# Performance work log

Measured on AMD Instinct MI355X. Metric: run time of the kernel, lower is better.

Reference implementation:

```python
import jax, jax.numpy as jnp
import numpy as np

N_LEVELS = 16
N_FEATS = 2
MIN_RES = 16
MAX_RES = 2048
LOG2_T = 19
T = 1 << LOG2_T  # 524288 hash-table entries per level
B = np.exp((np.log(MAX_RES) - np.log(MIN_RES)) / (N_LEVELS - 1))  # per-level scale ~1.3819
PRIME_Y = np.uint32(2654435761)  # tcnn 2D spatial-hash prime (x prime is 1)
MASK = jnp.uint32(T - 1)


def hash_encode(uv, table):
    """Multiresolution hash-grid encoding (tcnn HashGrid, 2D, bilinear).
    uv: [N,2] in [0,1); table: [L,T,F]. Returns [N, L*F]."""
    outs = []
    for l in range(N_LEVELS):
        scale = MIN_RES * (B ** l) - 1.0          # tcnn grid_scale
        res = int(np.ceil(scale)) + 1             # tcnn grid_resolution
        dense = (res * res) <= T                  # small levels are dense grids
        pos = uv * jnp.float32(scale) + jnp.float32(0.5)
        pg_f = jnp.floor(pos)
        frac = pos - pg_f                          # [N,2] bilinear weights
        pg = pg_f.astype(jnp.uint32)

        def corner_idx(ox, oy):
            x = pg[:, 0] + jnp.uint32(ox)
            y = pg[:, 1] + jnp.uint32(oy)
            if dense:
                return (x + y * jnp.uint32(res)) & MASK
            return (x ^ (y * PRIME_Y)) & MASK

        fx = frac[:, 0:1]
        fy = frac[:, 1:2]
        tl = table[l]
        feat = ((1.0 - fx) * (1.0 - fy) * tl[corner_idx(0, 0)]
                + fx * (1.0 - fy) * tl[corner_idx(1, 0)]
                + (1.0 - fx) * fy * tl[corner_idx(0, 1)]
                + fx * fy * tl[corner_idx(1, 1)])
        outs.append(feat)
    return jnp.concatenate(outs, axis=-1)  # [N, 32]


def mlp(x, w0, w1, w2):
    # FullyFusedMLP: no biases, ReLU hidden, Sigmoid output
    h = jax.nn.relu(x @ w0)
    h = jax.nn.relu(h @ w1)
    return jax.nn.sigmoid(h @ w2)  # [N, 3]


def setup_inputs() -> dict:
    key = jax.random.key(0)
    ks = jax.random.split(key, 5)
    N = 2_097_152
    uv = jax.random.uniform(ks[0], (N, 2), jnp.float32)
    # tcnn HashGrid init: uniform in [-1e-4, 1e-4]
    table = jax.random.uniform(ks[1], (N_LEVELS, T, N_FEATS), jnp.float32, -1e-4, 1e-4)
    w0 = jax.random.normal(ks[2], (32, 64), jnp.float32) * jnp.float32(1.0 / np.sqrt(32))
    w1 = jax.random.normal(ks[3], (64, 64), jnp.float32) * jnp.float32(1.0 / np.sqrt(64))
    w2 = jax.random.normal(ks[4], (64, 3), jnp.float32) * jnp.float32(1.0 / np.sqrt(64))
    return {"uv": uv, "table": table, "w0": w0, "w1": w1, "w2": w2}


def reference(uv, table, w0, w1, w2):
    return mlp(hash_encode(uv, table), w0, w1, w2)
```

## Files before the change

kernel.cpp:

```cpp
#include <hip/hip_runtime.h>
#include <math.h>
#include <stdint.h>

#define NLV 16
#define LOG2T 19
#define TSZ (1u << LOG2T)
#define TMASK (TSZ - 1u)
#define PRIME_Y 2654435761u

#define NFRAG 14
#define WPF_USHORTS (NFRAG * 64 * 8)

#define NCOARSE 512
#define P1_PTS 8192
#define P2_CAP 5120

struct NGPParams {
    float scale[NLV];
    unsigned res[NLV];
    unsigned hashed_mask;
};

struct __align__(8) pairld { float x, y, z, w; };

typedef __attribute__((ext_vector_type(8))) short bf16x8;
typedef __attribute__((ext_vector_type(4))) float f32x4;

__device__ inline ushort bf16_rn(float f) {
    uint32_t u = __float_as_uint(f);
    return (ushort)((u + 0x7FFFu + ((u >> 16) & 1u)) >> 16);
}
__device__ inline uint32_t pack_bf16(float a, float b) {
    uint32_t ua = __float_as_uint(a);
    uint32_t ub = __float_as_uint(b);
    uint32_t lo = (ua + 0x7FFFu + ((ua >> 16) & 1u)) >> 16;
    uint32_t hi = (ub + 0x7FFFu + ((ub >> 16) & 1u)) & 0xFFFF0000u;
    return lo | hi;
}
__device__ inline uint32_t pack_trunc(float a, float b) {
    return __builtin_amdgcn_perm(__float_as_uint(a), __float_as_uint(b), 0x07060302u);
}
__device__ inline unsigned coarse_of(float2 v) {
    unsigned b = (unsigned)(v.y * 512.f); return b > 511u ? 511u : b;
}
__device__ inline unsigned fine_of(float2 v) {
    unsigned b = (unsigned)(v.x * 256.f); return b > 255u ? 255u : b;
}
__device__ inline int xcd_swz(int orig, int nwg) {
    const int q = nwg >> 3, r = nwg & 7;
    const int xcd = orig & 7, k = orig >> 3;
    return (xcd < r ? xcd * (q + 1) : r * (q + 1) + (xcd - r) * q) + k;
}

__global__ __launch_bounds__(256) void ngp_prep_wfrag(
    const float* __restrict__ w0, const float* __restrict__ w1,
    const float* __restrict__ w2, ushort* __restrict__ wpf)
{
    const int t = threadIdx.x;
    for (int i = 0; i < 4; ++i) {
        const int e = t + 256 * i;
        if (e >= NFRAG * 64) continue;
        const int f = e >> 6, lane = e & 63;
        const int g4 = lane >> 4, r16 = lane & 15;
        ushort v[8];
        if (f < 4) {
            const int n = f * 16 + r16, k0 = 8 * g4;
            #pragma unroll
            for (int j = 0; j < 8; ++j) v[j] = bf16_rn(w0[(k0 + j) * 64 + n]);
        } else if (f < 12) {
            const int q = f - 4;
            const int n = (q >> 1) * 16 + r16, k0 = (q & 1) * 32 + 8 * g4;
            #pragma unroll
            for (int j = 0; j < 8; ++j) v[j] = bf16_rn(w1[(k0 + j) * 64 + n]);
        } else {
            const int n = r16, k0 = (f - 12) * 32 + 8 * g4;
            #pragma unroll
            for (int j = 0; j < 8; ++j)
                v[j] = (n < 3) ? bf16_rn(w2[(k0 + j) * 3 + n]) : (ushort)0;
        }
        #pragma unroll
        for (int j = 0; j < 8; ++j) wpf[e * 8 + j] = v[j];
    }
}

__global__ __launch_bounds__(1024) void ngp_hist512(
    const float2* __restrict__ uv, uint32_t* __restrict__ hist, int n)
{
    __shared__ unsigned int h[NCOARSE];
    const int t = threadIdx.x;
    if (t < NCOARSE) h[t] = 0;
    __syncthreads();
    const int b0 = blockIdx.x * P1_PTS;
    #pragma unroll
    for (int k = 0; k < 8; ++k) {
        const int i = b0 + t + k * 1024;
        if (i < n) atomicAdd(&h[coarse_of(uv[i])], 1u);
    }
    __syncthreads();
    if (t < NCOARSE && h[t]) atomicAdd(&hist[t], h[t]);
}

__global__ __launch_bounds__(512) void ngp_scan512(
    const uint32_t* __restrict__ hist, uint32_t* __restrict__ base,
    uint32_t* __restrict__ cursor)
{
    __shared__ unsigned int s[NCOARSE];
    const int t = threadIdx.x;
    const uint32_t mine = hist[t];
    s[t] = mine;
    __syncthreads();
    for (int off = 1; off < NCOARSE; off <<= 1) {
        uint32_t v = (t >= off) ? s[t - off] : 0u;
        __syncthreads();
        s[t] += v;
        __syncthreads();
    }
    const uint32_t excl = s[t] - mine;
    base[t] = excl;
    cursor[t] = excl;
}

__global__ __launch_bounds__(1024) void ngp_pass1(
    const float2* __restrict__ uv, uint32_t* __restrict__ cursor,
    float2* __restrict__ suv, uint32_t* __restrict__ perm, int n)
{
    __shared__ float2       spt[P1_PTS];
    __shared__ unsigned int sid[P1_PTS];
    __shared__ unsigned int hist[NCOARSE], lbase[NCOARSE], lcur[NCOARSE], gbase[NCOARSE];
    __shared__ unsigned int stot;

    const int t = threadIdx.x;
    const int b0 = blockIdx.x * P1_PTS;
    if (t < NCOARSE) hist[t] = 0;
    __syncthreads();

    float2 p[8]; unsigned pc[8];
    #pragma unroll
    for (int k = 0; k < 8; ++k) {
        const int i = b0 + t + k * 1024;
        if (i < n) {
            p[k] = uv[i];
            pc[k] = coarse_of(p[k]);
            atomicAdd(&hist[pc[k]], 1u);
        } else pc[k] = 0xFFFFFFFFu;
    }
    __syncthreads();
    if (t < NCOARSE) lbase[t] = hist[t];
    __syncthreads();
    for (int off = 1; off < NCOARSE; off <<= 1) {
        uint32_t v = 0;
        if (t < NCOARSE && t >= off) v = lbase[t - off];
        __syncthreads();
        if (t < NCOARSE) lbase[t] += v;
        __syncthreads();
    }
    if (t < NCOARSE) {
        const uint32_t excl = lbase[t] - hist[t];
        lcur[t] = excl;
        gbase[t] = atomicAdd(&cursor[t], hist[t]);
        lbase[t] = excl;
        if (t == NCOARSE - 1) stot = excl + hist[t];
    }
    __syncthreads();
    #pragma unroll
    for (int k = 0; k < 8; ++k) {
        if (pc[k] != 0xFFFFFFFFu) {
            const uint32_t r = atomicAdd(&lcur[pc[k]], 1u);
            spt[r] = p[k];
            sid[r] = (unsigned)(b0 + t + k * 1024);
        }
    }
    __syncthreads();
    const uint32_t tot = stot;
    for (uint32_t j = t; j < tot; j += 1024) {
        const float2 v = spt[j];
        const unsigned c = coarse_of(v);
        const uint32_t d = gbase[c] + (j - lbase[c]);
        suv[d] = v;
        perm[d] = sid[j];
    }
}

__global__ __launch_bounds__(1024) void ngp_pass2(
    const uint32_t* __restrict__ basev, const uint32_t* __restrict__ histv,
    float2* __restrict__ suv, uint32_t* __restrict__ perm)
{
    __shared__ float2       spt[P2_CAP];
    __shared__ unsigned int sid[P2_CAP];
    __shared__ unsigned int hist[256], lbase[256], lcur[256];

    const int b = blockIdx.x;
    const uint32_t lo = basev[b];
    const uint32_t cnt = histv[b];
    if (cnt > P2_CAP) return;
    const int t = threadIdx.x;
    if (t < 256) hist[t] = 0;
    __syncthreads();
    for (uint32_t j = t; j < cnt; j += 1024) {
        const float2 v = suv[lo + j];
        spt[j] = v; sid[j] = perm[lo + j];
        atomicAdd(&hist[fine_of(v)], 1u);
    }
    __syncthreads();
    if (t < 256) lbase[t] = hist[t];
    __syncthreads();
    for (int off = 1; off < 256; off <<= 1) {
        uint32_t v = 0;
        if (t < 256 && t >= off) v = lbase[t - off];
        __syncthreads();
        if (t < 256) lbase[t] += v;
        __syncthreads();
    }
    if (t < 256) lcur[t] = lbase[t] - hist[t];
    __syncthreads();
    for (uint32_t j = t; j < cnt; j += 1024) {
        const float2 v = spt[j];
        const uint32_t r = atomicAdd(&lcur[fine_of(v)], 1u);
        suv[lo + r] = v;
        perm[lo + r] = sid[j];
    }
}

__global__ __launch_bounds__(256) void ngp_encode2_kernel(
    const float2* __restrict__ pts,
    const float2* __restrict__ table,
    uint32_t* __restrict__ xt,
    NGPParams p, int n, int chunks2)
{
    const int bid = blockIdx.x;
    const int pass = bid / chunks2;
    const int chunk = xcd_swz(bid - pass * chunks2, chunks2);
    const int base = chunk * 512 + threadIdx.x;

    float2 xy[2];
    #pragma unroll
    for (int q = 0; q < 2; ++q) {
        int idx = base + q * 256;
        xy[q] = pts[idx < n ? idx : (n - 1)];
    }

    const int l0 = (pass == 0) ? 0 : (pass == 1 ? 10 : 10 + pass);
    const int l1 = (pass == 0) ? 9 : (pass == 1 ? 11 : 10 + pass);

    for (int l = l0; l <= l1; ++l) {
        const float s = p.scale[l];
        const unsigned res = p.res[l];
        const bool hashed = (p.hashed_mask >> l) & 1u;
        const float2* tl = table + ((size_t)l << LOG2T);

        #pragma unroll
        for (int q = 0; q < 2; ++q) {
            const float px = xy[q].x * s + 0.5f;
            const float py = xy[q].y * s + 0.5f;
            const float fpx = floorf(px), fpy = floorf(py);
            const float fx = px - fpx, fy = py - fpy;
            const unsigned x0 = (unsigned)fpx, y0 = (unsigned)fpy;

            float2 c00, c10, c01, c11;
            if (!hashed) {
                const unsigned b0 = x0 + y0 * res;
                const pairld q0 = *(const pairld*)(tl + b0);
                const pairld q1 = *(const pairld*)(tl + b0 + res);
                c00 = make_float2(q0.x, q0.y); c10 = make_float2(q0.z, q0.w);
                c01 = make_float2(q1.x, q1.y); c11 = make_float2(q1.z, q1.w);
            } else {
                const unsigned hy0 = y0 * PRIME_Y;
                const unsigned hy1 = (y0 + 1u) * PRIME_Y;
                if (!(x0 & 1u)) {
                    const unsigned i0 = (x0 ^ hy0) & TMASK;
                    const unsigned i2 = (x0 ^ hy1) & TMASK;
                    const pairld q0 = *(const pairld*)(tl + (i0 & ~1u));
                    const pairld q2 = *(const pairld*)(tl + (i2 & ~1u));
                    if (i0 & 1u) { c00 = make_float2(q0.z, q0.w); c10 = make_float2(q0.x, q0.y); }
                    else         { c00 = make_float2(q0.x, q0.y); c10 = make_float2(q0.z, q0.w); }
                    if (i2 & 1u) { c01 = make_float2(q2.z, q2.w); c11 = make_float2(q2.x, q2.y); }
                    else         { c01 = make_float2(q2.x, q2.y); c11 = make_float2(q2.z, q2.w); }
                } else {
                    c00 = tl[(x0 ^ hy0) & TMASK];
                    c10 = tl[((x0 + 1u) ^ hy0) & TMASK];
                    c01 = tl[(x0 ^ hy1) & TMASK];
                    c11 = tl[((x0 + 1u) ^ hy1) & TMASK];
                }
            }

            const float w00 = (1.f - fx) * (1.f - fy);
            const float w10 = fx * (1.f - fy);
            const float w01 = (1.f - fx) * fy;
            const float w11 = fx * fy;
            const float f0 = w00 * c00.x + w10 * c10.x + w01 * c01.x + w11 * c11.x;
            const float f1 = w00 * c00.y + w10 * c10.y + w01 * c01.y + w11 * c11.y;
            const int idx = base + q * 256;
            if (idx < n) xt[(size_t)l * n + idx] = pack_bf16(f0, f1);
        }
    }
}

__global__ __launch_bounds__(256, 4) void ngp_mlp_persist(
    const uint32_t* __restrict__ xt,
    const ushort* __restrict__ wpf,
    const uint32_t* __restrict__ perm,
    float* __restrict__ out, int n, int nchunks)
{
    __shared__ __align__(16) ushort H[256 * 72];

    const int t = threadIdx.x;
    const int lane = t & 63;
    const int w = t >> 6;
    const int g4 = lane >> 4;
    const int r16 = lane & 15;

    bf16x8 wf[NFRAG];
    #pragma unroll
    for (int f = 0; f < NFRAG; ++f)
        wf[f] = *(const bf16x8*)(wpf + (size_t)(f * 64 + lane) * 8);

    for (int c = blockIdx.x; c < nchunks; c += gridDim.x) {
        const int pbase = c << 8;
        #pragma unroll
        for (int mi = 0; mi < 4; ++mi) {
            const int plocal = (w * 4 + mi) * 16 + r16;
            int pg = pbase + plocal;
            pg = pg < n ? pg : n - 1;
            union { uint32_t u[4]; bf16x8 v; } cv;
            #pragma unroll
            for (int c4 = 0; c4 < 4; ++c4)
                cv.u[c4] = xt[(size_t)(4 * g4 + c4) * n + pg];
            f32x4 a[4];
            #pragma unroll
            for (int nt = 0; nt < 4; ++nt)
                a[nt] = __builtin_amdgcn_mfma_f32_16x16x32_bf16(
                    wf[nt], cv.v, (f32x4){0.f, 0.f, 0.f, 0.f}, 0, 0, 0);
            const int pl = plocal * 72;
            #pragma unroll
            for (int nt = 0; nt < 4; ++nt) {
                const uint32_t d0 = pack_trunc(fmaxf(a[nt][1], 0.f), fmaxf(a[nt][0], 0.f));
                const uint32_t d1 = pack_trunc(fmaxf(a[nt][3], 0.f), fmaxf(a[nt][2], 0.f));
                *(uint2*)&H[pl + nt * 16 + 4 * g4] = make_uint2(d0, d1);
            }
        }
        #pragma unroll
        for (int mi = 0; mi < 4; ++mi) {
            const int plocal = (w * 4 + mi) * 16 + r16;
            const int pl = plocal * 72;
            const bf16x8 bh0 = *(const bf16x8*)&H[pl + 8 * g4];
            const bf16x8 bh1 = *(const bf16x8*)&H[pl + 32 + 8 * g4];
            #pragma unroll
            for (int nt = 0; nt < 4; ++nt) {
                f32x4 acc = __builtin_amdgcn_mfma_f32_16x16x32_bf16(
                    wf[4 + nt * 2], bh0, (f32x4){0.f, 0.f, 0.f, 0.f}, 0, 0, 0);
                acc = __builtin_amdgcn_mfma_f32_16x16x32_bf16(
                    wf[4 + nt * 2 + 1], bh1, acc, 0, 0, 0);
                const uint32_t d0 = pack_trunc(fmaxf(acc[1], 0.f), fmaxf(acc[0], 0.f));
                const uint32_t d1 = pack_trunc(fmaxf(acc[3], 0.f), fmaxf(acc[2], 0.f));
                *(uint2*)&H[pl + nt * 16 + 4 * g4] = make_uint2(d0, d1);
            }
            const bf16x8 ch0 = *(const bf16x8*)&H[pl + 8 * g4];
            const bf16x8 ch1 = *(const bf16x8*)&H[pl + 32 + 8 * g4];
            f32x4 z = __builtin_amdgcn_mfma_f32_16x16x32_bf16(
                wf[12], ch0, (f32x4){0.f, 0.f, 0.f, 0.f}, 0, 0, 0);
            z = __builtin_amdgcn_mfma_f32_16x16x32_bf16(wf[13], ch1, z, 0, 0, 0);
            if (g4 == 0) {
                const int pgs = pbase + plocal;
                if (pgs < n) {
                    const int pg = perm ? (int)perm[pgs] : pgs;
                    #pragma unroll
                    for (int r = 0; r < 3; ++r)
                        out[(size_t)pg * 3 + r] = 1.f / (1.f + __expf(-z[r]));
                }
            }
        }
    }
}

__global__ __launch_bounds__(256) void ngp_fused_kernel(
    const float2* __restrict__ uv,
    const float2* __restrict__ table,
    const float4* __restrict__ w0,
    const float4* __restrict__ w1,
    const float*  __restrict__ w2,
    float* __restrict__ out,
    NGPParams p, int n)
{
    __shared__ float4 sw0[512];
    __shared__ float4 sw1[1024];
    __shared__ float  sw2[192];
    const int t = threadIdx.x;
    #pragma unroll
    for (int i = 0; i < 2; i++) sw0[t + 256 * i] = w0[t + 256 * i];
    #pragma unroll
    for (int i = 0; i < 4; i++) sw1[t + 256 * i] = w1[t + 256 * i];
    if (t < 192) sw2[t] = w2[t];
    __syncthreads();
    const int gi = blockIdx.x * 256 + t;
    if (gi >= n) return;
    const float2 xy = uv[gi];
    float feat[32];
    #pragma unroll
    for (int l = 0; l < NLV; l++) {
        const float s = p.scale[l];
        const unsigned res = p.res[l];
        const float px = xy.x * s + 0.5f;
        const float py = xy.y * s + 0.5f;
        const float fpx = floorf(px), fpy = floorf(py);
        const float fx = px - fpx, fy = py - fpy;
        const unsigned x0 = (unsigned)fpx, y0 = (unsigned)fpy;
        unsigned i00, i10, i01, i11;
        if (!((p.hashed_mask >> l) & 1u)) {
            const unsigned b = x0 + y0 * res;
            i00 = b & TMASK; i10 = (b + 1u) & TMASK;
            i01 = (b + res) & TMASK; i11 = (b + res + 1u) & TMASK;
        } else {
            const unsigned hy0 = y0 * PRIME_Y;
            const unsigned hy1 = (y0 + 1u) * PRIME_Y;
            i00 = (x0 ^ hy0) & TMASK; i10 = ((x0 + 1u) ^ hy0) & TMASK;
            i01 = (x0 ^ hy1) & TMASK; i11 = ((x0 + 1u) ^ hy1) & TMASK;
        }
        const float2* tl = table + ((size_t)l << LOG2T);
        const float2 c00 = tl[i00], c10 = tl[i10], c01 = tl[i01], c11 = tl[i11];
        const float w00 = (1.f - fx) * (1.f - fy);
        const float w10 = fx * (1.f - fy);
        const float w01 = (1.f - fx) * fy;
        const float w11 = fx * fy;
        feat[2 * l]     = w00 * c00.x + w10 * c10.x + w01 * c01.x + w11 * c11.x;
        feat[2 * l + 1] = w00 * c00.y + w10 * c10.y + w01 * c01.y + w11 * c11.y;
    }
    float2 h0[32];
    #pragma unroll
    for (int j = 0; j < 32; j++) h0[j] = make_float2(0.f, 0.f);
    #pragma unroll
    for (int k = 0; k < 32; k++) {
        const float f = feat[k];
        #pragma unroll
        for (int j = 0; j < 16; j++) {
            const float4 ww = sw0[k * 16 + j];
            h0[2 * j].x = fmaf(f, ww.x, h0[2 * j].x);
            h0[2 * j].y = fmaf(f, ww.y, h0[2 * j].y);
            h0[2 * j + 1].x = fmaf(f, ww.z, h0[2 * j + 1].x);
            h0[2 * j + 1].y = fmaf(f, ww.w, h0[2 * j + 1].y);
        }
    }
    #pragma unroll
    for (int j = 0; j < 32; j++) {
        h0[j].x = fmaxf(h0[j].x, 0.f);
        h0[j].y = fmaxf(h0[j].y, 0.f);
    }
    float2 h1[32];
    #pragma unroll
    for (int j = 0; j < 32; j++) h1[j] = make_float2(0.f, 0.f);
    #pragma unroll
    for (int k = 0; k < 64; k++) {
        const float f = (k & 1) ? h0[k >> 1].y : h0[k >> 1].x;
        #pragma unroll
        for (int j = 0; j < 16; j++) {
            const float4 ww = sw1[k * 16 + j];
            h1[2 * j].x = fmaf(f, ww.x, h1[2 * j].x);
            h1[2 * j].y = fmaf(f, ww.y, h1[2 * j].y);
            h1[2 * j + 1].x = fmaf(f, ww.z, h1[2 * j + 1].x);
            h1[2 * j + 1].y = fmaf(f, ww.w, h1[2 * j + 1].y);
        }
    }
    #pragma unroll
    for (int j = 0; j < 32; j++) {
        h1[j].x = fmaxf(h1[j].x, 0.f);
        h1[j].y = fmaxf(h1[j].y, 0.f);
    }
    float z0 = 0.f, z1 = 0.f, z2 = 0.f;
    #pragma unroll
    for (int k = 0; k < 64; k++) {
        const float f = (k & 1) ? h1[k >> 1].y : h1[k >> 1].x;
        z0 = fmaf(f, sw2[3 * k + 0], z0);
        z1 = fmaf(f, sw2[3 * k + 1], z1);
        z2 = fmaf(f, sw2[3 * k + 2], z2);
    }
    out[3 * gi + 0] = 1.f / (1.f + __expf(-z0));
    out[3 * gi + 1] = 1.f / (1.f + __expf(-z1));
    out[3 * gi + 2] = 1.f / (1.f + __expf(-z2));
}

extern "C" void kernel_launch(void* const* d_in, const int* in_sizes, int n_in,
                              void* d_out, int out_size, void* d_ws, size_t ws_size,
                              hipStream_t stream) {
    const float2* uv    = (const float2*)d_in[0];
    const float2* table = (const float2*)d_in[1];
    const float*  w0f   = (const float*)d_in[2];
    const float*  w1f   = (const float*)d_in[3];
    const float*  w2f   = (const float*)d_in[4];
    float* out = (float*)d_out;

    const int n = in_sizes[0] / 2;

    NGPParams p;
    p.hashed_mask = 0;
    const double B = exp((log(2048.0) - log(16.0)) / 15.0);
    for (int l = 0; l < NLV; l++) {
        const double scale = 16.0 * pow(B, (double)l) - 1.0;
        const long long res = (long long)ceil(scale) + 1;
        p.scale[l] = (float)scale;
        p.res[l] = (unsigned)res;
        if (res * res > (long long)TSZ) p.hashed_mask |= (1u << l);
    }

    const size_t xt_bytes   = (size_t)NLV * (size_t)n * 4u;
    const size_t wpf_bytes  = ((size_t)WPF_USHORTS * 2u + 63u) & ~63ull;
    const size_t suv_bytes  = (size_t)n * 8u;
    const size_t perm_bytes = (size_t)n * 4u;
    const size_t ctl_bytes  = (size_t)NCOARSE * 4u * 3u;

    const size_t need_sorted = xt_bytes + wpf_bytes + suv_bytes + perm_bytes + ctl_bytes;
    const size_t need_plain  = xt_bytes + wpf_bytes;

    const int chunks  = (n + 255) / 256;
    const int chunks2 = (n + 511) / 512;

    if (ws_size < need_plain) {
        ngp_fused_kernel<<<chunks, 256, 0, stream>>>(
            uv, table, (const float4*)w0f, (const float4*)w1f, w2f, out, p, n);
        return;
    }

    uint32_t* xt  = (uint32_t*)d_ws;
    ushort*   wpf = (ushort*)((char*)d_ws + xt_bytes);
    ngp_prep_wfrag<<<1, 256, 0, stream>>>(w0f, w1f, w2f, wpf);

    const int mlp_blocks = chunks < 1024 ? chunks : 1024;

    if (ws_size < need_sorted) {
        ngp_encode2_kernel<<<6 * chunks2, 256, 0, stream>>>(uv, table, xt, p, n, chunks2);
        ngp_mlp_persist<<<mlp_blocks, 256, 0, stream>>>(xt, wpf, (const uint32_t*)nullptr, out, n, chunks);
        return;
    }

    float2*   suv    = (float2*)((char*)d_ws + xt_bytes + wpf_bytes);
    uint32_t* perm   = (uint32_t*)((char*)suv + suv_bytes);
    uint32_t* hist   = (uint32_t*)((char*)perm + perm_bytes);
    uint32_t* basev  = hist + NCOARSE;
    uint32_t* cursor = basev + NCOARSE;

    const int p1_blocks = (n + P1_PTS - 1) / P1_PTS;

    hipMemsetAsync(hist, 0, (size_t)NCOARSE * 4u, stream);
    ngp_hist512<<<p1_blocks, 1024, 0, stream>>>(uv, hist, n);
    ngp_scan512<<<1, NCOARSE, 0, stream>>>(hist, basev, cursor);
    ngp_pass1<<<p1_blocks, 1024, 0, stream>>>(uv, cursor, suv, perm, n);
    ngp_pass2<<<NCOARSE, 1024, 0, stream>>>(basev, hist, suv, perm);
    ngp_encode2_kernel<<<6 * chunks2, 256, 0, stream>>>(suv, table, xt, p, n, chunks2);
    ngp_mlp_persist<<<mlp_blocks, 256, 0, stream>>>(xt, wpf, perm, out, n, chunks);
}
```

Measured before the change: 189.6 us.

## Store encoded features as scaled FP8 and use FP8 MFMA for first layer

The intermediate encoded-feature buffer changes from packed bf16 pairs to packed FP8 pairs, with features pre-scaled by 8192 so the tiny hash-table values fall in FP8 range. The first MLP layer uses FP8 MFMA with FP8 weights, and the scale is undone before ReLU. This halves the intermediate buffer's write and read traffic between the encode and MLP kernels. The cost is a large loss of precision in the features and first-layer weights, which risks exceeding the accuracy tolerance.

```diff
diff --git a/kernel.cpp b/kernel.cpp
--- a/kernel.cpp
+++ b/kernel.cpp
@@ -8,8 +8,12 @@
 #define TMASK (TSZ - 1u)
 #define PRIME_Y 2654435761u
 
-#define NFRAG 14
-#define WPF_USHORTS (NFRAG * 64 * 8)
+#define WP8_BYTES  (4 * 64 * 8)
+#define WP16_BYTES (10 * 64 * 16)
+#define WPF_BYTES  (WP8_BYTES + WP16_BYTES)
+
+#define FSCALE 8192.0f
+#define FUNSCALE (1.0f / 8192.0f)
 
 #define NCOARSE 512
 #define P1_PTS 8192
@@ -30,15 +34,13 @@
     uint32_t u = __float_as_uint(f);
     return (ushort)((u + 0x7FFFu + ((u >> 16) & 1u)) >> 16);
 }
-__device__ inline uint32_t pack_bf16(float a, float b) {
-    uint32_t ua = __float_as_uint(a);
-    uint32_t ub = __float_as_uint(b);
-    uint32_t lo = (ua + 0x7FFFu + ((ua >> 16) & 1u)) >> 16;
-    uint32_t hi = (ub + 0x7FFFu + ((ub >> 16) & 1u)) & 0xFFFF0000u;
-    return lo | hi;
-}
 __device__ inline uint32_t pack_trunc(float a, float b) {
     return __builtin_amdgcn_perm(__float_as_uint(a), __float_as_uint(b), 0x07060302u);
+}
+__device__ inline ushort cvt_pk_fp8(float a, float b) {
+    unsigned r = 0;
+    asm("v_cvt_pk_fp8_f32 %0, %1, %2" : "+v"(r) : "v"(a), "v"(b));
+    return (ushort)r;
 }
 __device__ inline unsigned coarse_of(float2 v) {
     unsigned b = (unsigned)(v.y * 512.f); return b > 511u ? 511u : b;
@@ -54,32 +56,41 @@
 
 __global__ __launch_bounds__(256) void ngp_prep_wfrag(
     const float* __restrict__ w0, const float* __restrict__ w1,
-    const float* __restrict__ w2, ushort* __restrict__ wpf)
-{
-    const int t = threadIdx.x;
-    for (int i = 0; i < 4; ++i) {
+    const float* __restrict__ w2,
+    unsigned long long* __restrict__ wp8, ushort* __restrict__ wp16)
+{
+    const int t = threadIdx.x;
+    {
+        const int f = t >> 6, lane = t & 63;
+        const int g4 = lane >> 4, r16 = lane & 15;
+        const int nn = f * 16 + r16, k0 = 8 * g4;
+        float v[8];
+        #pragma unroll
+        for (int j = 0; j < 8; ++j) v[j] = w0[(k0 + j) * 64 + nn];
+        const unsigned long long p0 = cvt_pk_fp8(v[0], v[1]);
+        const unsigned long long p1 = cvt_pk_fp8(v[2], v[3]);
+        const unsigned long long p2 = cvt_pk_fp8(v[4], v[5]);
+        const unsigned long long p3 = cvt_pk_fp8(v[6], v[7]);
+        wp8[f * 64 + lane] = p0 | (p1 << 16) | (p2 << 32) | (p3 << 48);
+    }
+    for (int i = 0; i < 3; ++i) {
         const int e = t + 256 * i;
-        if (e >= NFRAG * 64) continue;
+        if (e >= 640) continue;
         const int f = e >> 6, lane = e & 63;
         const int g4 = lane >> 4, r16 = lane & 15;
         ushort v[8];
-        if (f < 4) {
-            const int n = f * 16 + r16, k0 = 8 * g4;
+        if (f < 8) {
+            const int nn = (f >> 1) * 16 + r16, k0 = (f & 1) * 32 + 8 * g4;
             #pragma unroll
-            for (int j = 0; j < 8; ++j) v[j] = bf16_rn(w0[(k0 + j) * 64 + n]);
-        } else if (f < 12) {
-            const int q = f - 4;
-            const int n = (q >> 1) * 16 + r16, k0 = (q & 1) * 32 + 8 * g4;
-            #pragma unroll
-            for (int j = 0; j < 8; ++j) v[j] = bf16_rn(w1[(k0 + j) * 64 + n]);
+            for (int j = 0; j < 8; ++j) v[j] = bf16_rn(w1[(k0 + j) * 64 + nn]);
         } else {
-            const int n = r16, k0 = (f - 12) * 32 + 8 * g4;
+            const int nn = r16, k0 = (f - 8) * 32 + 8 * g4;
             #pragma unroll
             for (int j = 0; j < 8; ++j)
-                v[j] = (n < 3) ? bf16_rn(w2[(k0 + j) * 3 + n]) : (ushort)0;
-        }
-        #pragma unroll
-        for (int j = 0; j < 8; ++j) wpf[e * 8 + j] = v[j];
+                v[j] = (nn < 3) ? bf16_rn(w2[(k0 + j) * 3 + nn]) : (ushort)0;
+        }
+        #pragma unroll
+        for (int j = 0; j < 8; ++j) wp16[e * 8 + j] = v[j];
     }
 }
 
@@ -224,7 +235,7 @@
 __global__ __launch_bounds__(256) void ngp_encode2_kernel(
     const float2* __restrict__ pts,
     const float2* __restrict__ table,
-    uint32_t* __restrict__ xt,
+    ushort* __restrict__ xt,
     NGPParams p, int n, int chunks2)
 {
     const int bid = blockIdx.x;
@@ -289,15 +300,17 @@
             const float w11 = fx * fy;
             const float f0 = w00 * c00.x + w10 * c10.x + w01 * c01.x + w11 * c11.x;
             const float f1 = w00 * c00.y + w10 * c10.y + w01 * c01.y + w11 * c11.y;
+            const ushort pk = cvt_pk_fp8(f0 * FSCALE, f1 * FSCALE);
             const int idx = base + q * 256;
-            if (idx < n) xt[(size_t)l * n + idx] = pack_bf16(f0, f1);
+            if (idx < n) xt[(size_t)l * n + idx] = pk;
         }
     }
 }
 
 __global__ __launch_bounds__(256, 4) void ngp_mlp_persist(
-    const uint32_t* __restrict__ xt,
-    const ushort* __restrict__ wpf,
+    const ushort* __restrict__ xt,
+    const unsigned long long* __restrict__ wp8,
+    const ushort* __restrict__ wp16,
     const uint32_t* __restrict__ perm,
     float* __restrict__ out, int n, int nchunks)
 {
@@ -309,10 +322,13 @@
     const int g4 = lane >> 4;
     const int r16 = lane & 15;
 
-    bf16x8 wf[NFRAG];
-    #pragma unroll
-    for (int f = 0; f < NFRAG; ++f)
-        wf[f] = *(const bf16x8*)(wpf + (size_t)(f * 64 + lane) * 8);
+    unsigned long long wf8[4];
+    #pragma unroll
+    for (int f = 0; f < 4; ++f) wf8[f] = wp8[f * 64 + lane];
+    bf16x8 wf16[10];
+    #pragma unroll
+    for (int f = 0; f < 10; ++f)
+        wf16[f] = *(const bf16x8*)(wp16 + (size_t)(f * 64 + lane) * 8);
 
     for (int c = blockIdx.x; c < nchunks; c += gridDim.x) {
         const int pbase = c << 8;
@@ -321,20 +337,22 @@
             const int plocal = (w * 4 + mi) * 16 + r16;
             int pg = pbase + plocal;
             pg = pg < n ? pg : n - 1;
-            union { uint32_t u[4]; bf16x8 v; } cv;
+            union { ushort s[4]; unsigned long long v; } xv;
             #pragma unroll
             for (int c4 = 0; c4 < 4; ++c4)
-                cv.u[c4] = xt[(size_t)(4 * g4 + c4) * n + pg];
+                xv.s[c4] = xt[(size_t)(4 * g4 + c4) * n + pg];
             f32x4 a[4];
             #pragma unroll
             for (int nt = 0; nt < 4; ++nt)
-                a[nt] = __builtin_amdgcn_mfma_f32_16x16x32_bf16(
-                    wf[nt], cv.v, (f32x4){0.f, 0.f, 0.f, 0.f}, 0, 0, 0);
+                a[nt] = __builtin_amdgcn_mfma_f32_16x16x32_fp8_fp8(
+                    (long)wf8[nt], (long)xv.v, (f32x4){0.f, 0.f, 0.f, 0.f}, 0, 0, 0);
             const int pl = plocal * 72;
             #pragma unroll
             for (int nt = 0; nt < 4; ++nt) {
-                const uint32_t d0 = pack_trunc(fmaxf(a[nt][1], 0.f), fmaxf(a[nt][0], 0.f));
-                const uint32_t d1 = pack_trunc(fmaxf(a[nt][3], 0.f), fmaxf(a[nt][2], 0.f));
+                const uint32_t d0 = pack_trunc(fmaxf(a[nt][1] * FUNSCALE, 0.f),
+                                               fmaxf(a[nt][0] * FUNSCALE, 0.f));
+                const uint32_t d1 = pack_trunc(fmaxf(a[nt][3] * FUNSCALE, 0.f),
+                                               fmaxf(a[nt][2] * FUNSCALE, 0.f));
                 *(uint2*)&H[pl + nt * 16 + 4 * g4] = make_uint2(d0, d1);
             }
         }
@@ -347,9 +365,9 @@
             #pragma unroll
             for (int nt = 0; nt < 4; ++nt) {
                 f32x4 acc = __builtin_amdgcn_mfma_f32_16x16x32_bf16(
-                    wf[4 + nt * 2], bh0, (f32x4){0.f, 0.f, 0.f, 0.f}, 0, 0, 0);
+                    wf16[nt * 2], bh0, (f32x4){0.f, 0.f, 0.f, 0.f}, 0, 0, 0);
                 acc = __builtin_amdgcn_mfma_f32_16x16x32_bf16(
-                    wf[4 + nt * 2 + 1], bh1, acc, 0, 0, 0);
+                    wf16[nt * 2 + 1], bh1, acc, 0, 0, 0);
                 const uint32_t d0 = pack_trunc(fmaxf(acc[1], 0.f), fmaxf(acc[0], 0.f));
                 const uint32_t d1 = pack_trunc(fmaxf(acc[3], 0.f), fmaxf(acc[2], 0.f));
                 *(uint2*)&H[pl + nt * 16 + 4 * g4] = make_uint2(d0, d1);
@@ -357,8 +375,8 @@
             const bf16x8 ch0 = *(const bf16x8*)&H[pl + 8 * g4];
             const bf16x8 ch1 = *(const bf16x8*)&H[pl + 32 + 8 * g4];
             f32x4 z = __builtin_amdgcn_mfma_f32_16x16x32_bf16(
-                wf[12], ch0, (f32x4){0.f, 0.f, 0.f, 0.f}, 0, 0, 0);
-            z = __builtin_amdgcn_mfma_f32_16x16x32_bf16(wf[13], ch1, z, 0, 0, 0);
+                wf16[8], ch0, (f32x4){0.f, 0.f, 0.f, 0.f}, 0, 0, 0);
+            z = __builtin_amdgcn_mfma_f32_16x16x32_bf16(wf16[9], ch1, z, 0, 0, 0);
             if (g4 == 0) {
                 const int pgs = pbase + plocal;
                 if (pgs < n) {
@@ -500,8 +518,8 @@
         if (res * res > (long long)TSZ) p.hashed_mask |= (1u << l);
     }
 
-    const size_t xt_bytes   = (size_t)NLV * (size_t)n * 4u;
-    const size_t wpf_bytes  = ((size_t)WPF_USHORTS * 2u + 63u) & ~63ull;
+    const size_t xt_bytes   = (size_t)NLV * (size_t)n * 2u;
+    const size_t wpf_bytes  = ((size_t)WPF_BYTES + 63u) & ~63ull;
     const size_t suv_bytes  = (size_t)n * 8u;
     const size_t perm_bytes = (size_t)n * 4u;
     const size_t ctl_bytes  = (size_t)NCOARSE * 4u * 3u;
@@ -518,15 +536,17 @@
         return;
     }
 
-    uint32_t* xt  = (uint32_t*)d_ws;
-    ushort*   wpf = (ushort*)((char*)d_ws + xt_bytes);
-    ngp_prep_wfrag<<<1, 256, 0, stream>>>(w0f, w1f, w2f, wpf);
+    ushort* xt = (ushort*)d_ws;
+    unsigned long long* wp8 = (unsigned long long*)((char*)d_ws + xt_bytes);
+    ushort* wp16 = (ushort*)((char*)d_ws + xt_bytes + WP8_BYTES);
+    ngp_prep_wfrag<<<1, 256, 0, stream>>>(w0f, w1f, w2f, wp8, wp16);
 
     const int mlp_blocks = chunks < 1024 ? chunks : 1024;
 
     if (ws_size < need_sorted) {
         ngp_encode2_kernel<<<6 * chunks2, 256, 0, stream>>>(uv, table, xt, p, n, chunks2);
-        ngp_mlp_persist<<<mlp_blocks, 256, 0, stream>>>(xt, wpf, (const uint32_t*)nullptr, out, n, chunks);
+        ngp_mlp_persist<<<mlp_blocks, 256, 0, stream>>>(xt, wp8, wp16,
+                                                        (const uint32_t*)nullptr, out, n, chunks);
         return;
     }
 
@@ -544,5 +564,5 @@
     ngp_pass1<<<p1_blocks, 1024, 0, stream>>>(uv, cursor, suv, perm, n);
     ngp_pass2<<<NCOARSE, 1024, 0, stream>>>(basev, hist, suv, perm);
     ngp_encode2_kernel<<<6 * chunks2, 256, 0, stream>>>(suv, table, xt, p, n, chunks2);
-    ngp_mlp_persist<<<mlp_blocks, 256, 0, stream>>>(xt, wpf, perm, out, n, chunks);
-}
+    ngp_mlp_persist<<<mlp_blocks, 256, 0, stream>>>(xt, wp8, wp16, perm, out, n, chunks);
+}
```

Result: faster. 175.6 us (-7.4%).
